# Kernel tuning notes

Measured on AMD Instinct MI355X. Metric: run time of the kernel, lower is better.

Reference implementation:

```python
import jax, jax.numpy as jnp
import numpy as np

N_NODES = 50000
N_EDGES = 800000
D_IN = 128
HIDDEN = 128
N_GRAPHS = 256
N_CLASSES = 10
NEG_SLOPE = 0.2


def gatv2_conv(x, src, dst, Wl, Wr, att, bias, num_nodes):
    # PyG GATv2Conv, heads=1, add_self_loops handled by caller via src/dst.
    xl = x @ Wl  # [N, H] source transform
    xr = x @ Wr  # [N, H] target transform
    # per-edge attention logits: a^T LeakyReLU(xl[src] + xr[dst])
    e = jax.nn.leaky_relu(xl[src] + xr[dst], NEG_SLOPE) @ att  # [E]
    # segment softmax over incoming edges of each dst node
    e_max = jax.ops.segment_max(e, dst, num_segments=num_nodes)
    e_exp = jnp.exp(e - e_max[dst])
    denom = jax.ops.segment_sum(e_exp, dst, num_segments=num_nodes)
    alpha = e_exp / (denom[dst] + 1e-16)  # [E]
    out = jax.ops.segment_sum(alpha[:, None] * xl[src], dst, num_segments=num_nodes)
    return out + bias


def setup_inputs() -> dict:
    key = jax.random.key(0)
    ks = jax.random.split(key, 12)
    x = jax.random.normal(ks[0], (N_NODES, D_IN), dtype=jnp.float32)
    edge_index = jax.random.randint(ks[1], (2, N_EDGES), 0, N_NODES, dtype=jnp.int64)
    batch = jnp.sort(jax.random.randint(ks[2], (N_NODES,), 0, N_GRAPHS, dtype=jnp.int64))
    s = 1.0 / np.sqrt(D_IN)
    sh = 1.0 / np.sqrt(HIDDEN)
    return {
        "x": x, "edge_index": edge_index, "batch": batch,
        "Wl1": jax.random.normal(ks[3], (D_IN, HIDDEN), jnp.float32) * s,
        "Wr1": jax.random.normal(ks[4], (D_IN, HIDDEN), jnp.float32) * s,
        "att1": jax.random.normal(ks[5], (HIDDEN,), jnp.float32) * sh,
        "b1": jnp.zeros((HIDDEN,), jnp.float32),
        "g_ln": jnp.ones((HIDDEN,), jnp.float32),
        "b_ln": jnp.zeros((HIDDEN,), jnp.float32),
        "Wl2": jax.random.normal(ks[6], (HIDDEN, HIDDEN), jnp.float32) * sh,
        "Wr2": jax.random.normal(ks[7], (HIDDEN, HIDDEN), jnp.float32) * sh,
        "att2": jax.random.normal(ks[8], (HIDDEN,), jnp.float32) * sh,
        "b2": jnp.zeros((HIDDEN,), jnp.float32),
        "Wlin": jax.random.normal(ks[9], (HIDDEN, N_CLASSES), jnp.float32) * sh,
        "blin": jnp.zeros((N_CLASSES,), jnp.float32),
    }


def reference(x, edge_index, batch, Wl1, Wr1, att1, b1, g_ln, b_ln,
              Wl2, Wr2, att2, b2, Wlin, blin):
    n = x.shape[0]
    # add self loops (PyG GATv2Conv default add_self_loops=True)
    loops = jnp.arange(n, dtype=edge_index.dtype)
    src = jnp.concatenate([edge_index[0], loops])
    dst = jnp.concatenate([edge_index[1], loops])

    h = gatv2_conv(x, src, dst, Wl1, Wr1, att1, b1, n)
    h = jax.nn.relu(h)
    # layer norm over feature dim
    mu = jnp.mean(h, axis=-1, keepdims=True)
    var = jnp.var(h, axis=-1, keepdims=True)
    h = (h - mu) * jax.lax.rsqrt(var + 1e-5) * g_ln + b_ln

    h = gatv2_conv(h, src, dst, Wl2, Wr2, att2, b2, n)

    # global mean pool per graph
    sums = jax.ops.segment_sum(h, batch, num_segments=N_GRAPHS)
    cnts = jax.ops.segment_sum(jnp.ones((n,), h.dtype), batch, num_segments=N_GRAPHS)
    pooled = sums / jnp.maximum(cnts, 1.0)[:, None]
    # dropout p=0.4 is identity in eval mode
    return pooled @ Wlin + blin
```

## Files before the change

kernel.cpp:

```cpp
#include <hip/hip_runtime.h>
#include <hip/hip_bf16.h>
#include <hip/hip_fp16.h>

#define NN 50000
#define NE 800000
#define HID 128
#define NG 256
#define NC 10
#define NB 196
#define CHUNK 4096
#define BCAP 8192

using half8  = __attribute__((ext_vector_type(8))) _Float16;
using half2v = __attribute__((ext_vector_type(2))) _Float16;
using f32x4  = __attribute__((ext_vector_type(4))) float;

__device__ __forceinline__ float fdot2f(unsigned a, unsigned b, float c)
{
#if __has_builtin(__builtin_amdgcn_fdot2)
    return __builtin_amdgcn_fdot2(*(half2v*)&a, *(half2v*)&b, c, false);
#else
    float2 fa = __half22float2(*(__half2*)&a);
    float2 fb = __half22float2(*(__half2*)&b);
    return fmaf(fa.x, fb.x, fmaf(fa.y, fb.y, c));
#endif
}

__device__ __forceinline__ unsigned addleaky_h2(unsigned xl, unsigned xr)
{
    half2v s = *(half2v*)&xl + *(half2v*)&xr;
    half2v l = __builtin_elementwise_max(s, s * (_Float16)0.2f);
    return *(unsigned*)&l;
}

__global__ __launch_bounds__(256) void k_wpackz(
    const float* __restrict__ Wl1, const float* __restrict__ Wr1,
    const float* __restrict__ Wl2, const float* __restrict__ Wr2,
    __half* __restrict__ wpk1, __half* __restrict__ wpk2,
    float* __restrict__ pooled, float* __restrict__ cnt,
    int* __restrict__ cursor)
{
    int gidx = blockIdx.x * 256 + threadIdx.x;
#pragma unroll
    for (int i = 0; i < 4; i++) pooled[gidx + i * 8192] = 0.f;
    if (gidx < NG) cnt[gidx] = 0.f;
    else if (gidx < NG + 256) cursor[gidx - NG] = 0;

    int idx = gidx & 4095;
    int layer = gidx >> 12;
    const float* Wl = layer ? Wl2 : Wl1;
    const float* Wr = layer ? Wr2 : Wr1;
    __half* wpk = layer ? wpk2 : wpk1;

    int t = idx >> 8;
    int lane = idx & 63;
    const float* W = (t < 8) ? Wl : Wr;
    int col = ((t & 7) << 4) + (lane & 15);
    int k0 = (((idx >> 6) & 3) << 5) + ((lane >> 4) << 3);
    __half tmp[8];
#pragma unroll
    for (int j = 0; j < 8; j++)
        tmp[j] = __float2half(W[(size_t)(k0 + j) * 128 + col]);
    *(uint4*)(wpk + ((size_t)idx << 3)) = *(uint4*)tmp;
}

template <bool F32IN>
__global__ __launch_bounds__(256) void k_mgemm(
    const void* __restrict__ in, const __half* __restrict__ wpk,
    __half* __restrict__ xlh, __half* __restrict__ xrh)
{
    const int w = threadIdx.x >> 6;
    const int lane = threadIdx.x & 63;
    const int nodebase = blockIdx.x * 64 + w * 16;
    const int lrow = lane & 15;
    const int kb = lane >> 4;

    const int nload = min(nodebase + lrow, NN - 1);

    half8 a[4];
    if constexpr (F32IN) {
        const float* xp = (const float*)in + (size_t)nload * 128 + (kb << 3);
#pragma unroll
        for (int kf = 0; kf < 4; kf++) {
            float4 f0 = *(const float4*)(xp + kf * 32);
            float4 f1 = *(const float4*)(xp + kf * 32 + 4);
            half8 hh;
            hh[0] = (_Float16)f0.x; hh[1] = (_Float16)f0.y;
            hh[2] = (_Float16)f0.z; hh[3] = (_Float16)f0.w;
            hh[4] = (_Float16)f1.x; hh[5] = (_Float16)f1.y;
            hh[6] = (_Float16)f1.z; hh[7] = (_Float16)f1.w;
            a[kf] = hh;
        }
    } else {
        const char* xp = (const char*)in + (size_t)nload * 256 + (kb << 4);
#pragma unroll
        for (int kf = 0; kf < 4; kf++) {
            uint4 u = *(const uint4*)(xp + kf * 64);
            a[kf] = *(half8*)&u;
        }
    }

    const uint4* wp = (const uint4*)wpk + lane;

#pragma unroll
    for (int t = 0; t < 16; t++) {
        f32x4 acc = {0.f, 0.f, 0.f, 0.f};
#pragma unroll
        for (int kf = 0; kf < 4; kf++) {
            uint4 bu = wp[(t * 4 + kf) * 64];
            half8 b = *(half8*)&bu;
            acc = __builtin_amdgcn_mfma_f32_16x16x32_f16(a[kf], b, acc, 0, 0, 0);
        }
        int col = ((t & 7) << 4) + lrow;
#pragma unroll
        for (int i = 0; i < 4; i++) {
            int node = nodebase + kb * 4 + i;
            if (node < NN) {
                if (t < 8) xlh[(size_t)node * 128 + col] = __float2half(acc[i]);
                else       xrh[(size_t)node * 128 + col] = __float2half(acc[i]);
            }
        }
    }
}

__device__ __forceinline__ int block_scan_incl(int v, int t)
{
    __shared__ int sm[256];
    sm[t] = v;
    __syncthreads();
#pragma unroll
    for (int off = 1; off < 256; off <<= 1) {
        int u = (t >= off) ? sm[t - off] : 0;
        __syncthreads();
        sm[t] += u;
        __syncthreads();
    }
    return sm[t];
}

__global__ __launch_bounds__(256) void k_bscatter(
    const int* __restrict__ ei, int* __restrict__ cursor,
    unsigned* __restrict__ pairbuf)
{
    __shared__ int lcnt[256], cstart[256], lcur[256], gpos[256];
    __shared__ unsigned sorted[CHUNK];
    __shared__ unsigned char sortedB[CHUNK];
    const int t = threadIdx.x;
    const int base = blockIdx.x * CHUNK;
    const int n = min(CHUNK, NE - base);
    if (n <= 0) return;

    lcnt[t] = 0;
    __syncthreads();

    unsigned pk[16];
    int bk[16];
#pragma unroll
    for (int i = 0; i < 16; i++) {
        int off = i * 256 + t;
        bk[i] = -1;
        if (off < n) {
            int e = base + off;
            int s = ei[e], d = ei[NE + e];
            bk[i] = d >> 8;
            pk[i] = ((unsigned)s << 8) | (unsigned)(d & 255);
            atomicAdd(&lcnt[bk[i]], 1);
        }
    }
    __syncthreads();

    int v = lcnt[t];
    int inc = block_scan_incl(v, t);
    cstart[t] = inc - v;
    lcur[t] = inc - v;
    __syncthreads();
    gpos[t] = (v > 0) ? atomicAdd(&cursor[t], v) : 0;
    __syncthreads();

#pragma unroll
    for (int i = 0; i < 16; i++) {
        if (bk[i] >= 0) {
            int r = atomicAdd(&lcur[bk[i]], 1);
            sorted[r] = pk[i];
            sortedB[r] = (unsigned char)bk[i];
        }
    }
    __syncthreads();

    for (int j = t; j < n; j += 256) {
        int b = sortedB[j];
        pairbuf[(size_t)b * BCAP + gpos[b] + (j - cstart[b])] = sorted[j];
    }
}

__global__ __launch_bounds__(256) void k_bbuild(
    const unsigned* __restrict__ pairbuf, const int* __restrict__ cursor,
    int* __restrict__ rowptr, int* __restrict__ esrc)
{
    __shared__ int pre[256];
    __shared__ int ncnt[256], cur[256];
    const int b = blockIdx.x;
    const int t = threadIdx.x;
    const int node0 = b * 256;
    const int nnodes = min(256, NN - node0);

    int cb = (t < NB) ? cursor[t] : 0;
    int nodes = (t < NB) ? min(256, NN - t * 256) : 0;
    int inc = block_scan_incl(cb + nodes, t);
    pre[t] = inc;
    __syncthreads();
    const int row0 = (b == 0) ? 0 : pre[b - 1];
    const int cnt = cursor[b];
    const unsigned* pb = pairbuf + (size_t)b * BCAP;

    ncnt[t] = 0;
    __syncthreads();
    for (int i = t; i < cnt; i += 256)
        atomicAdd(&ncnt[pb[i] & 255u], 1);
    __syncthreads();

    int v = (t < nnodes) ? ncnt[t] + 1 : 0;
    int inc2 = block_scan_incl(v, t);
    int rb = row0 + inc2 - v;
    if (t < nnodes) {
        rowptr[node0 + t] = rb;
        esrc[rb] = node0 + t;
        cur[t] = rb + 1;
    }
    if (b == NB - 1 && t == 0) rowptr[NN] = NE + NN;
    __syncthreads();

    for (int i = t; i < cnt; i += 256) {
        unsigned p = pb[i];
        int pos = atomicAdd(&cur[p & 255u], 1);
        esrc[pos] = (int)(p >> 8);
    }
}

#define GAT_LOGIT(A, e)                                                     \
    {                                                                       \
        unsigned l0 = addleaky_h2(A.x, xrq.x);                              \
        unsigned l1 = addleaky_h2(A.y, xrq.y);                              \
        unsigned l2 = addleaky_h2(A.z, xrq.z);                              \
        unsigned l3 = addleaky_h2(A.w, xrq.w);                              \
        e = fdot2f(l0, atq.x, 0.f);                                         \
        e = fdot2f(l1, atq.y, e);                                           \
        e = fdot2f(l2, atq.z, e);                                           \
        e = fdot2f(l3, atq.w, e);                                           \
        _Pragma("unroll")                                                   \
        for (int off = 8; off; off >>= 1) e += __shfl_xor(e, off, 64);      \
    }

#define GAT_ACC(A, p)                                                       \
    {                                                                       \
        half8 ah = *(half8*)&A;                                             \
        _Pragma("unroll")                                                   \
        for (int i = 0; i < 8; i++)                                         \
            acc[i] = fmaf(p, (float)ah[i], acc[i]);                         \
    }

__device__ __forceinline__ void gat_core(
    const char* __restrict__ xlb, const int* __restrict__ esrc,
    int beg, int end, int lane, const uint4 xrq, const uint4 atq,
    float* acc, float& den)
{
    const int g = lane >> 4;
    const unsigned qb = (unsigned)((lane & 15) << 4);
#pragma unroll
    for (int i = 0; i < 8; i++) acc[i] = 0.f;
    den = 0.f;

    for (int sc = beg; sc < end; sc += 64) {
        const int nv = min(end - sc, 64);
        const int nit = (nv + 3) >> 2;
        const int nfull = nv >> 2;
        int myidx = esrc[sc + lane] & 0xFFFF;

        auto LD = [&](int j) -> uint4 {
            int t = (j << 2) + g;
            int s = __shfl(myidx, t, 64);
            unsigned off = ((unsigned)s << 8) | qb;
            return *(const uint4*)(xlb + off);
        };

        uint4 A = LD(0);
        uint4 B = LD(1 < nit ? 1 : 0);

#pragma unroll 2
        for (int jj = 0; jj < nfull; ++jj) {
            uint4 C = LD(jj + 2 < nit ? jj + 2 : nit - 1);
            float e;
            GAT_LOGIT(A, e)
            float p = __expf(fminf(e, 80.f));
            den += p;
            GAT_ACC(A, p)
            A = B; B = C;
        }
        if (nv & 3) {
            float e;
            GAT_LOGIT(A, e)
            float p = ((nfull << 2) + g < nv) ? __expf(fminf(e, 80.f)) : 0.f;
            den += p;
            GAT_ACC(A, p)
        }
    }

#pragma unroll
    for (int off = 16; off < 64; off <<= 1) {
        den += __shfl_xor(den, off, 64);
#pragma unroll
        for (int i = 0; i < 8; i++) acc[i] += __shfl_xor(acc[i], off, 64);
    }
}

__device__ __forceinline__ uint4 ld_att_h2(const float* att, int q)
{
    float4 c = *(const float4*)(att + q * 8);
    float4 e = *(const float4*)(att + q * 8 + 4);
    __half2 t0 = __floats2half2_rn(c.x, c.y);
    __half2 t1 = __floats2half2_rn(c.z, c.w);
    __half2 t2 = __floats2half2_rn(e.x, e.y);
    __half2 t3 = __floats2half2_rn(e.z, e.w);
    uint4 r;
    r.x = *(unsigned*)&t0; r.y = *(unsigned*)&t1;
    r.z = *(unsigned*)&t2; r.w = *(unsigned*)&t3;
    return r;
}

__global__ __launch_bounds__(256, 8) void k_gat1(
    const char* __restrict__ xlb, const char* __restrict__ xrb,
    const float* __restrict__ att, const int* __restrict__ rowptr,
    const int* __restrict__ esrc, const float* __restrict__ bias,
    const float* __restrict__ g_ln, const float* __restrict__ b_ln,
    char* __restrict__ h16b)
{
    int d = (int)((blockIdx.x * 256 + threadIdx.x) >> 6);
    int lane = threadIdx.x & 63;
    int q = lane & 15;

    uint4 xrq = *(const uint4*)(xrb + ((size_t)d << 8) + (q << 4));
    uint4 atq = ld_att_h2(att, q);

    float acc[8]; float den;
    gat_core(xlb, esrc, rowptr[d], rowptr[d + 1], lane, xrq, atq, acc, den);

    float inv = 1.f / (den + 1e-16f);
    float x[8];
    {
        float4 a = *(const float4*)(bias + q * 8);
        float4 b = *(const float4*)(bias + q * 8 + 4);
        float bb[8] = {a.x,a.y,a.z,a.w,b.x,b.y,b.z,b.w};
#pragma unroll
        for (int i = 0; i < 8; i++) x[i] = fmaxf(fmaf(acc[i], inv, bb[i]), 0.f);
    }

    float s1 = 0.f, s2 = 0.f;
#pragma unroll
    for (int i = 0; i < 8; i++) { s1 += x[i]; s2 += x[i] * x[i]; }
#pragma unroll
    for (int off = 8; off; off >>= 1) {
        s1 += __shfl_xor(s1, off, 64);
        s2 += __shfl_xor(s2, off, 64);
    }
    float mu = s1 * (1.f / 128.f);
    float var = s2 * (1.f / 128.f) - mu * mu;
    float rstd = rsqrtf(var + 1e-5f);

    if (lane < 16) {
        float4 ga = *(const float4*)(g_ln + q * 8);
        float4 gb = *(const float4*)(g_ln + q * 8 + 4);
        float4 ba = *(const float4*)(b_ln + q * 8);
        float4 bb = *(const float4*)(b_ln + q * 8 + 4);
        float o[8];
        o[0] = (x[0]-mu)*rstd*ga.x + ba.x;
        o[1] = (x[1]-mu)*rstd*ga.y + ba.y;
        o[2] = (x[2]-mu)*rstd*ga.z + ba.z;
        o[3] = (x[3]-mu)*rstd*ga.w + ba.w;
        o[4] = (x[4]-mu)*rstd*gb.x + bb.x;
        o[5] = (x[5]-mu)*rstd*gb.y + bb.y;
        o[6] = (x[6]-mu)*rstd*gb.z + bb.z;
        o[7] = (x[7]-mu)*rstd*gb.w + bb.w;
        __half2 p0 = __floats2half2_rn(o[0], o[1]);
        __half2 p1 = __floats2half2_rn(o[2], o[3]);
        __half2 p2 = __floats2half2_rn(o[4], o[5]);
        __half2 p3 = __floats2half2_rn(o[6], o[7]);
        uint4 u;
        u.x = *(unsigned*)&p0; u.y = *(unsigned*)&p1;
        u.z = *(unsigned*)&p2; u.w = *(unsigned*)&p3;
        *(uint4*)(h16b + ((size_t)d << 8) + (q << 4)) = u;
    }
}

__global__ __launch_bounds__(256, 8) void k_gat2(
    const char* __restrict__ xlb, const char* __restrict__ xrb,
    const float* __restrict__ att, const int* __restrict__ rowptr,
    const int* __restrict__ esrc, const float* __restrict__ bias,
    char* __restrict__ h2b)
{
    int d = (int)((blockIdx.x * 256 + threadIdx.x) >> 6);
    int lane = threadIdx.x & 63;
    int q = lane & 15;

    uint4 xrq = *(const uint4*)(xrb + ((size_t)d << 8) + (q << 4));
    uint4 atq = ld_att_h2(att, q);

    float acc[8]; float den;
    gat_core(xlb, esrc, rowptr[d], rowptr[d + 1], lane, xrq, atq, acc, den);

    float inv = 1.f / (den + 1e-16f);
    if (lane < 16) {
        float4 a = *(const float4*)(bias + q * 8);
        float4 b = *(const float4*)(bias + q * 8 + 4);
        float o[8];
        o[0] = fmaf(acc[0], inv, a.x);
        o[1] = fmaf(acc[1], inv, a.y);
        o[2] = fmaf(acc[2], inv, a.z);
        o[3] = fmaf(acc[3], inv, a.w);
        o[4] = fmaf(acc[4], inv, b.x);
        o[5] = fmaf(acc[5], inv, b.y);
        o[6] = fmaf(acc[6], inv, b.z);
        o[7] = fmaf(acc[7], inv, b.w);
        __half2 p0 = __floats2half2_rn(o[0], o[1]);
        __half2 p1 = __floats2half2_rn(o[2], o[3]);
        __half2 p2 = __floats2half2_rn(o[4], o[5]);
        __half2 p3 = __floats2half2_rn(o[6], o[7]);
        uint4 u;
        u.x = *(unsigned*)&p0; u.y = *(unsigned*)&p1;
        u.z = *(unsigned*)&p2; u.w = *(unsigned*)&p3;
        *(uint4*)(h2b + ((size_t)d << 8) + (q << 4)) = u;
    }
}

#define NPB 100
__global__ __launch_bounds__(128) void k_pool(
    const __half* __restrict__ h2h, const int* __restrict__ batch,
    float* __restrict__ pooled, float* __restrict__ cnt)
{
    int n0 = blockIdx.x * NPB;
    int n1 = min(n0 + NPB, NN);
    if (n0 >= NN) return;
    int f = threadIdx.x;

    float s = 0.f;
    int c = 0;
    int curg = batch[n0];
    for (int n = n0; n < n1; n++) {
        int g = batch[n];
        if (g != curg) {
            atomicAdd(pooled + (size_t)curg * 128 + f, s);
            if (f == 0) atomicAdd(cnt + curg, (float)c);
            s = 0.f; c = 0; curg = g;
        }
        s += __half2float(h2h[(size_t)n * 128 + f]);
        c++;
    }
    atomicAdd(pooled + (size_t)curg * 128 + f, s);
    if (f == 0) atomicAdd(cnt + curg, (float)c);
}

__global__ __launch_bounds__(256) void k_linear(
    const float* __restrict__ pooled, const float* __restrict__ cnt,
    const float* __restrict__ W, const float* __restrict__ b,
    float* __restrict__ out)
{
    int idx = blockIdx.x * 256 + threadIdx.x;
    if (idx >= NG * NC) return;
    int g = idx / NC, c = idx % NC;
    float invc = 1.f / fmaxf(cnt[g], 1.f);
    float s = 0.f;
    for (int k = 0; k < HID; k++)
        s = fmaf(pooled[(size_t)g * 128 + k], W[(size_t)k * NC + c], s);
    out[idx] = fmaf(s, invc, b[c]);
}

extern "C" void kernel_launch(void* const* d_in, const int* in_sizes, int n_in,
                              void* d_out, int out_size, void* d_ws, size_t ws_size,
                              hipStream_t stream)
{
    const float* x     = (const float*)d_in[0];
    const int*   ei    = (const int*)d_in[1];
    const int*   batch = (const int*)d_in[2];
    const float* Wl1   = (const float*)d_in[3];
    const float* Wr1   = (const float*)d_in[4];
    const float* att1  = (const float*)d_in[5];
    const float* b1    = (const float*)d_in[6];
    const float* g_ln  = (const float*)d_in[7];
    const float* b_ln  = (const float*)d_in[8];
    const float* Wl2   = (const float*)d_in[9];
    const float* Wr2   = (const float*)d_in[10];
    const float* att2  = (const float*)d_in[11];
    const float* b2    = (const float*)d_in[12];
    const float* Wlin  = (const float*)d_in[13];
    const float* blin  = (const float*)d_in[14];
    float* out = (float*)d_out;

    char* ws = (char*)d_ws;
    __half* xlh16 = (__half*)ws;
    char*   xlb   = ws;
    __half* xrh16 = (__half*)(ws + (size_t)NN * 256);
    char*   xrb   = (char*)xrh16;
    __half* h16   = xrh16 + (size_t)NN * 128;
    __half* h2h   = h16 + (size_t)NN * 128;
    char*   h2b   = (char*)h2h;
    float* pooled = (float*)(h2h + (size_t)NN * 128);
    float* cnt    = pooled + (size_t)NG * HID;
    int* rowptr   = (int*)(cnt + NG);
    int* esrc     = rowptr + NN + 1;
    unsigned* pairbuf = (unsigned*)(esrc + NE + NN);
    int* cursor   = (int*)(pairbuf + (size_t)NB * BCAP);
    __half* wpk1  = (__half*)(cursor + 256);
    __half* wpk2  = wpk1 + 32768;

    const int mg_blocks  = (NN + 63) / 64;
    const int gat_blocks = (NN * 64) / 256;
    const int sc_blocks  = (NE + CHUNK - 1) / CHUNK;

    k_wpackz<<<32, 256, 0, stream>>>(Wl1, Wr1, Wl2, Wr2, wpk1, wpk2,
                                     pooled, cnt, cursor);

    k_bscatter<<<sc_blocks, 256, 0, stream>>>(ei, cursor, pairbuf);
    k_bbuild<<<NB, 256, 0, stream>>>(pairbuf, cursor, rowptr, esrc);

    k_mgemm<true><<<mg_blocks, 256, 0, stream>>>(x, wpk1, xlh16, xrh16);
    k_gat1<<<gat_blocks, 256, 0, stream>>>(xlb, xrb, att1, rowptr, esrc,
                                           b1, g_ln, b_ln, (char*)h16);

    k_mgemm<false><<<mg_blocks, 256, 0, stream>>>(h16, wpk2, xlh16, xrh16);
    k_gat2<<<gat_blocks, 256, 0, stream>>>(xlb, xrb, att2, rowptr, esrc,
                                           b2, h2b);

    k_pool<<<(NN + NPB - 1) / NPB, 128, 0, stream>>>(h2h, batch, pooled, cnt);
    k_linear<<<(NG * NC + 255) / 256, 256, 0, stream>>>(pooled, cnt, Wlin, blin, out);
}
```

Measured before the change: 191.0 us.

## Merge edge bucketing with first GEMM launch and fuse pooling with linear head

```diff
diff --git a/kernel.cpp b/kernel.cpp
--- a/kernel.cpp
+++ b/kernel.cpp
@@ -10,6 +10,8 @@
 #define NB 196
 #define CHUNK 4096
 #define BCAP 8192
+#define SCB 196
+#define MGB 782
 
 using half8  = __attribute__((ext_vector_type(8))) _Float16;
 using half2v = __attribute__((ext_vector_type(2))) _Float16;
@@ -37,14 +39,10 @@
     const float* __restrict__ Wl1, const float* __restrict__ Wr1,
     const float* __restrict__ Wl2, const float* __restrict__ Wr2,
     __half* __restrict__ wpk1, __half* __restrict__ wpk2,
-    float* __restrict__ pooled, float* __restrict__ cnt,
     int* __restrict__ cursor)
 {
     int gidx = blockIdx.x * 256 + threadIdx.x;
-#pragma unroll
-    for (int i = 0; i < 4; i++) pooled[gidx + i * 8192] = 0.f;
-    if (gidx < NG) cnt[gidx] = 0.f;
-    else if (gidx < NG + 256) cursor[gidx - NG] = 0;
+    if (gidx < 256) cursor[gidx] = 0;
 
     int idx = gidx & 4095;
     int layer = gidx >> 12;
@@ -65,13 +63,13 @@
 }
 
 template <bool F32IN>
-__global__ __launch_bounds__(256) void k_mgemm(
-    const void* __restrict__ in, const __half* __restrict__ wpk,
+__device__ __forceinline__ void mgemm_body(
+    int blk, const void* __restrict__ in, const __half* __restrict__ wpk,
     __half* __restrict__ xlh, __half* __restrict__ xrh)
 {
     const int w = threadIdx.x >> 6;
     const int lane = threadIdx.x & 63;
-    const int nodebase = blockIdx.x * 64 + w * 16;
+    const int nodebase = blk * 64 + w * 16;
     const int lrow = lane & 15;
     const int kb = lane >> 4;
 
@@ -138,15 +136,15 @@
     return sm[t];
 }
 
-__global__ __launch_bounds__(256) void k_bscatter(
-    const int* __restrict__ ei, int* __restrict__ cursor,
+__device__ __forceinline__ void bscatter_body(
+    int blk, const int* __restrict__ ei, int* __restrict__ cursor,
     unsigned* __restrict__ pairbuf)
 {
     __shared__ int lcnt[256], cstart[256], lcur[256], gpos[256];
     __shared__ unsigned sorted[CHUNK];
     __shared__ unsigned char sortedB[CHUNK];
     const int t = threadIdx.x;
-    const int base = blockIdx.x * CHUNK;
+    const int base = blk * CHUNK;
     const int n = min(CHUNK, NE - base);
     if (n <= 0) return;
 
@@ -191,6 +189,25 @@
         int b = sortedB[j];
         pairbuf[(size_t)b * BCAP + gpos[b] + (j - cstart[b])] = sorted[j];
     }
+}
+
+__global__ __launch_bounds__(256) void k_bscmg(
+    const int* __restrict__ ei, int* __restrict__ cursor,
+    unsigned* __restrict__ pairbuf, const float* __restrict__ x,
+    const __half* __restrict__ wpk1, __half* __restrict__ xlh,
+    __half* __restrict__ xrh)
+{
+    if (blockIdx.x < SCB)
+        bscatter_body(blockIdx.x, ei, cursor, pairbuf);
+    else
+        mgemm_body<true>(blockIdx.x - SCB, x, wpk1, xlh, xrh);
+}
+
+__global__ __launch_bounds__(256) void k_mgemm2(
+    const __half* __restrict__ in, const __half* __restrict__ wpk,
+    __half* __restrict__ xlh, __half* __restrict__ xrh)
+{
+    mgemm_body<false>(blockIdx.x, in, wpk, xlh, xrh);
 }
 
 __global__ __launch_bounds__(256) void k_bbuild(
@@ -431,46 +448,34 @@
     }
 }
 
-#define NPB 100
-__global__ __launch_bounds__(128) void k_pool(
+__global__ __launch_bounds__(128) void k_poolin(
     const __half* __restrict__ h2h, const int* __restrict__ batch,
-    float* __restrict__ pooled, float* __restrict__ cnt)
-{
-    int n0 = blockIdx.x * NPB;
-    int n1 = min(n0 + NPB, NN);
-    if (n0 >= NN) return;
-    int f = threadIdx.x;
-
-    float s = 0.f;
-    int c = 0;
-    int curg = batch[n0];
-    for (int n = n0; n < n1; n++) {
-        int g = batch[n];
-        if (g != curg) {
-            atomicAdd(pooled + (size_t)curg * 128 + f, s);
-            if (f == 0) atomicAdd(cnt + curg, (float)c);
-            s = 0.f; c = 0; curg = g;
-        }
-        s += __half2float(h2h[(size_t)n * 128 + f]);
-        c++;
-    }
-    atomicAdd(pooled + (size_t)curg * 128 + f, s);
-    if (f == 0) atomicAdd(cnt + curg, (float)c);
-}
-
-__global__ __launch_bounds__(256) void k_linear(
-    const float* __restrict__ pooled, const float* __restrict__ cnt,
     const float* __restrict__ W, const float* __restrict__ b,
     float* __restrict__ out)
 {
-    int idx = blockIdx.x * 256 + threadIdx.x;
-    if (idx >= NG * NC) return;
-    int g = idx / NC, c = idx % NC;
-    float invc = 1.f / fmaxf(cnt[g], 1.f);
+    const int g = blockIdx.x;
+    const int f = threadIdx.x;
+
+    int lo = 0, hi = NN;
+    while (lo < hi) { int m = (lo + hi) >> 1; if (batch[m] < g) lo = m + 1; else hi = m; }
+    int lo2 = lo, hi2 = NN;
+    while (lo2 < hi2) { int m = (lo2 + hi2) >> 1; if (batch[m] <= g) lo2 = m + 1; else hi2 = m; }
+
     float s = 0.f;
-    for (int k = 0; k < HID; k++)
-        s = fmaf(pooled[(size_t)g * 128 + k], W[(size_t)k * NC + c], s);
-    out[idx] = fmaf(s, invc, b[c]);
+    for (int n = lo; n < lo2; n++)
+        s += __half2float(h2h[(size_t)n * 128 + f]);
+
+    __shared__ float sm[128];
+    sm[f] = s;
+    __syncthreads();
+
+    if (f < NC) {
+        float invc = 1.f / fmaxf((float)(lo2 - lo), 1.f);
+        float a = 0.f;
+        for (int k = 0; k < HID; k++)
+            a = fmaf(sm[k], W[(size_t)k * NC + f], a);
+        out[(size_t)g * NC + f] = fmaf(a, invc, b[f]);
+    }
 }
 
 extern "C" void kernel_launch(void* const* d_in, const int* in_sizes, int n_in,
@@ -502,33 +507,29 @@
     __half* h16   = xrh16 + (size_t)NN * 128;
     __half* h2h   = h16 + (size_t)NN * 128;
     char*   h2b   = (char*)h2h;
-    float* pooled = (float*)(h2h + (size_t)NN * 128);
-    float* cnt    = pooled + (size_t)NG * HID;
-    int* rowptr   = (int*)(cnt + NG);
+    int* rowptr   = (int*)(h2h + (size_t)NN * 128);
     int* esrc     = rowptr + NN + 1;
     unsigned* pairbuf = (unsigned*)(esrc + NE + NN);
     int* cursor   = (int*)(pairbuf + (size_t)NB * BCAP);
     __half* wpk1  = (__half*)(cursor + 256);
     __half* wpk2  = wpk1 + 32768;
 
-    const int mg_blocks  = (NN + 63) / 64;
     const int gat_blocks = (NN * 64) / 256;
-    const int sc_blocks  = (NE + CHUNK - 1) / CHUNK;
-
-    k_wpackz<<<32, 256, 0, stream>>>(Wl1, Wr1, Wl2, Wr2, wpk1, wpk2,
-                                     pooled, cnt, cursor);
-
-    k_bscatter<<<sc_blocks, 256, 0, stream>>>(ei, cursor, pairbuf);
+
+    k_wpackz<<<32, 256, 0, stream>>>(Wl1, Wr1, Wl2, Wr2, wpk1, wpk2, cursor);
+
+    k_bscmg<<<SCB + MGB, 256, 0, stream>>>(ei, cursor, pairbuf, x, wpk1,
+                                           xlh16, xrh16);
+
     k_bbuild<<<NB, 256, 0, stream>>>(pairbuf, cursor, rowptr, esrc);
 
-    k_mgemm<true><<<mg_blocks, 256, 0, stream>>>(x, wpk1, xlh16, xrh16);
     k_gat1<<<gat_blocks, 256, 0, stream>>>(xlb, xrb, att1, rowptr, esrc,
                                            b1, g_ln, b_ln, (char*)h16);
 
-    k_mgemm<false><<<mg_blocks, 256, 0, stream>>>(h16, wpk2, xlh16, xrh16);
+    k_mgemm2<<<MGB, 256, 0, stream>>>(h16, wpk2, xlh16, xrh16);
+
     k_gat2<<<gat_blocks, 256, 0, stream>>>(xlb, xrb, att2, rowptr, esrc,
                                            b2, h2b);
 
-    k_pool<<<(NN + NPB - 1) / NPB, 128, 0, stream>>>(h2h, batch, pooled, cnt);
-    k_linear<<<(NG * NC + 255) / 256, 256, 0, stream>>>(pooled, cnt, Wlin, blin, out);
-}
+    k_poolin<<<NG, 128, 0, stream>>>(h2h, batch, Wlin, blin, out);
+}
```

After: 197.0 us. 3.2% more time.
